# Kernel optimization log

Measured on AMD Instinct MI355X. Metric: run time of the kernel, lower is better.

Reference implementation:

```python
import jax, jax.numpy as jnp
import numpy as np

N = 50000
E = 800000
D_IN = 128
D_HID = 128
D_EMB = 128
N_CLS = 3
EPS = 0.0  # GINConv default eps, not trainable here
LRELU_SLOPE = 0.2


def setup_inputs() -> dict:
    key = jax.random.key(0)
    ks = jax.random.split(key, 12)
    x = jax.random.normal(ks[0], (N, D_IN), dtype=jnp.float32)
    edge_index = jax.random.randint(ks[1], (2, E), 0, N, dtype=jnp.int64)
    node_label = jnp.zeros((10000, 1, N_CLS), dtype=jnp.float32)
    node_index = jax.random.randint(ks[2], (10000,), 0, N, dtype=jnp.int64)
    def lin(k, fan_in, fan_out):
        kw, kb = jax.random.split(k)
        bound = 1.0 / np.sqrt(fan_in)
        W = jax.random.uniform(kw, (fan_out, fan_in), minval=-bound, maxval=bound, dtype=jnp.float32)
        b = jax.random.uniform(kb, (fan_out,), minval=-bound, maxval=bound, dtype=jnp.float32)
        return W, b
    W1, b1 = lin(ks[3], D_IN, D_HID)
    W2, b2 = lin(ks[4], D_HID, D_HID)
    W3, b3 = lin(ks[5], D_HID, D_EMB)
    Wout, bout = lin(ks[6], D_EMB, N_CLS)
    return {"x": x, "edge_index": edge_index, "node_label": node_label,
            "node_index": node_index, "W1": W1, "b1": b1, "W2": W2, "b2": b2,
            "W3": W3, "b3": b3, "Wout": Wout, "bout": bout}


def gin_conv(x, src, dst, W, b):
    # h = Linear(x); out = relu(scatter_add(h[src] -> dst) + (1+eps)*h)
    h = x @ W.T + b                                   # [N, F_out]
    agg = jax.ops.segment_sum(h[src], dst, num_segments=N)
    return jax.nn.relu(agg + (1.0 + EPS) * h)


def leaky_relu(x):
    return jnp.where(x >= 0, x, LRELU_SLOPE * x)


def reference(x, edge_index, node_label, node_index, W1, b1, W2, b2, W3, b3, Wout, bout):
    src, dst = edge_index[0], edge_index[1]
    h = leaky_relu(gin_conv(x, src, dst, W1, b1))
    h = leaky_relu(gin_conv(h, src, dst, W2, b2))
    h = leaky_relu(gin_conv(h, src, dst, W3, b3))
    x_embed = h                                       # [N, D_EMB]
    output = h @ Wout.T + bout                        # [N, N_CLS]
    node_output = output[node_index]                  # [M, N_CLS]
    ypred = jnp.argmax(output, axis=1)                # [N]
    y_nodepred = ypred[node_index]                    # [M]
    return (x_embed, node_output, ypred, y_nodepred)
```

## Files before the change

kernel.cpp:

```cpp
#include <hip/hip_runtime.h>

#define NN 50000
#define EE 800000
#define D 128
#define NCLS 3
#define MIDX 10000
#define NB 196
#define CHUNK 4096
#define HIST_WGS 98
#define WCONV_WGS 64
#define LIN1_WGS 782

typedef unsigned int uint32;
typedef unsigned short ushort16;
typedef __attribute__((ext_vector_type(8))) short short8;
typedef __attribute__((ext_vector_type(4))) float f32x4;

__device__ __forceinline__ ushort16 f2bf(float f) {
    uint32 u = __float_as_uint(f);
    u = (u + 0x7fffu + ((u >> 16) & 1u)) >> 16;
    return (ushort16)u;
}
__device__ __forceinline__ float bflo(uint32 packed) {
    return __uint_as_float(packed << 16);
}
__device__ __forceinline__ float bfhi(uint32 packed) {
    return __uint_as_float(packed & 0xFFFF0000u);
}

__device__ __forceinline__ void gather_rows(const uint32* __restrict__ h,
                                            const int* __restrict__ esrc,
                                            int beg, int end, int lane,
                                            float& a0, float& a1) {
    int i = beg;
    for (; i + 16 <= end; i += 16) {
        int s[16];
        uint32 q[16];
#pragma unroll
        for (int k = 0; k < 16; ++k) s[k] = esrc[i + k];
#pragma unroll
        for (int k = 0; k < 16; ++k) q[k] = h[(long long)s[k] * (D / 2) + lane];
        float t0a = 0.f, t0b = 0.f, t1a = 0.f, t1b = 0.f;
#pragma unroll
        for (int k = 0; k < 16; k += 2) {
            t0a += bflo(q[k]);     t1a += bfhi(q[k]);
            t0b += bflo(q[k + 1]); t1b += bfhi(q[k + 1]);
        }
        a0 += t0a + t0b;
        a1 += t1a + t1b;
    }
    for (; i + 4 <= end; i += 4) {
        int s[4];
        uint32 q[4];
#pragma unroll
        for (int k = 0; k < 4; ++k) s[k] = esrc[i + k];
#pragma unroll
        for (int k = 0; k < 4; ++k) q[k] = h[(long long)s[k] * (D / 2) + lane];
        a0 += (bflo(q[0]) + bflo(q[1])) + (bflo(q[2]) + bflo(q[3]));
        a1 += (bfhi(q[0]) + bfhi(q[1])) + (bfhi(q[2]) + bfhi(q[3]));
    }
    for (; i < end; ++i) {
        const uint32 q = h[(long long)esrc[i] * (D / 2) + lane];
        a0 += bflo(q);
        a1 += bfhi(q);
    }
}


__global__ __launch_bounds__(256) void prep_hist(const float* __restrict__ W1,
                                                 const float* __restrict__ W2,
                                                 const float* __restrict__ W3,
                                                 const int* __restrict__ dst,
                                                 ushort16* __restrict__ Wbf,
                                                 int* __restrict__ hpart) {
    const int t = threadIdx.x;
    if (blockIdx.x < WCONV_WGS) {
        const int i = blockIdx.x * 256 + t;
        Wbf[i] = f2bf(W1[i]);
        Wbf[i + D * D] = f2bf(W2[i]);
        Wbf[i + 2 * D * D] = f2bf(W3[i]);
    } else {
        __shared__ int hcnt[256];
        const int b = blockIdx.x - WCONV_WGS;
        hcnt[t] = 0;
        __syncthreads();
        const int e0 = b * 8192;
        const int e1 = (e0 + 8192 < EE) ? e0 + 8192 : EE;
        for (int s = e0 + t; s < e1; s += 256) atomicAdd(&hcnt[dst[s] >> 8], 1);
        __syncthreads();
        hpart[b * 256 + t] = hcnt[t];
    }
}


__global__ __launch_bounds__(256) void scan_linear1(const int* __restrict__ hpart,
                                                    int* __restrict__ bstart,
                                                    int* __restrict__ bcursor,
                                                    int* __restrict__ rowptr,
                                                    const float* __restrict__ x,
                                                    const ushort16* __restrict__ Wbf,
                                                    const float* __restrict__ bias,
                                                    ushort16* __restrict__ h) {
    if (blockIdx.x == 0) {
        __shared__ int s[256];
        const int t = threadIdx.x;
        int v = 0;
        if (t < NB)
            for (int w = 0; w < HIST_WGS; ++w) v += hpart[w * 256 + t];
        s[t] = v;
        __syncthreads();
        for (int off = 1; off < 256; off <<= 1) {
            const int add = (t >= off) ? s[t - off] : 0;
            __syncthreads();
            s[t] += add;
            __syncthreads();
        }
        const int excl = s[t] - v;
        if (t < NB) {
            bstart[t] = excl;
            bcursor[t * 16] = excl;
        }
        if (t == NB - 1) bstart[NB] = excl + v;
        if (t == 0) rowptr[NN] = EE;
        return;
    }
    const int wave = threadIdx.x >> 6;
    const int lane = threadIdx.x & 63;
    const int m0 = (blockIdx.x - 1) * 64 + wave * 16;
    if (m0 >= NN) return;
    const int lr = lane & 15;
    const int lk = (lane >> 4) * 8;

    f32x4 acc[8] = {};
#pragma unroll
    for (int k4 = 0; k4 < 4; ++k4) {
        const int kb = k4 * 32 + lk;
        const float4* xp = (const float4*)(x + (long long)(m0 + lr) * D + kb);
        const float4 a0 = xp[0];
        const float4 a1 = xp[1];
        short8 af;
        af[0] = (short)f2bf(a0.x); af[1] = (short)f2bf(a0.y);
        af[2] = (short)f2bf(a0.z); af[3] = (short)f2bf(a0.w);
        af[4] = (short)f2bf(a1.x); af[5] = (short)f2bf(a1.y);
        af[6] = (short)f2bf(a1.z); af[7] = (short)f2bf(a1.w);
#pragma unroll
        for (int nt = 0; nt < 8; ++nt) {
            const short8 bfrag = *(const short8*)(Wbf + (nt * 16 + lr) * D + kb);
            acc[nt] = __builtin_amdgcn_mfma_f32_16x16x32_bf16(af, bfrag, acc[nt], 0, 0, 0);
        }
    }
    const int rbase = m0 + (lane >> 4) * 4;
#pragma unroll
    for (int nt = 0; nt < 8; ++nt) {
        const int f = nt * 16 + lr;
        const float bb = bias[f];
#pragma unroll
        for (int r = 0; r < 4; ++r)
            h[(long long)(rbase + r) * D + f] = f2bf(acc[nt][r] + bb);
    }
}


__global__ __launch_bounds__(256) void fill_coarse(const int* __restrict__ src,
                                                   const int* __restrict__ dst,
                                                   int* __restrict__ bcursor,
                                                   int* __restrict__ espacked) {
    __shared__ int hcnt[256];
    __shared__ int hbase[256];
    const int t = threadIdx.x;
    const int e0 = blockIdx.x * CHUNK;
    const int e1 = (e0 + CHUNK < EE) ? e0 + CHUNK : EE;
    hcnt[t] = 0;
    __syncthreads();
    for (int s = e0 + t; s < e1; s += 256) atomicAdd(&hcnt[dst[s] >> 8], 1);
    __syncthreads();
    if (t < NB) {
        const int c = hcnt[t];
        hbase[t] = c ? atomicAdd(&bcursor[t * 16], c) : 0;
    }
    hcnt[t] = 0;
    __syncthreads();
    for (int s = e0 + t; s < e1; s += 256) {
        const int d = dst[s];
        const int b = d >> 8;
        const int r = atomicAdd(&hcnt[b], 1);
        espacked[hbase[b] + r] = (src[s] << 8) | (d & 255);
    }
}


__global__ __launch_bounds__(256) void bucket_scatter(const int* __restrict__ espacked,
                                                      const int* __restrict__ bstart,
                                                      int* __restrict__ rowptr,
                                                      int* __restrict__ esrc) {
    __shared__ int cnt[256];
    __shared__ int sc[256];
    __shared__ int cur[256];
    const int b = blockIdx.x;
    const int t = threadIdx.x;
    const int n0 = b * 256;
    const int seg0 = bstart[b];
    const int seg1 = bstart[b + 1];
    cnt[t] = 0;
    __syncthreads();
    for (int s = seg0 + t; s < seg1; s += 256) atomicAdd(&cnt[espacked[s] & 255], 1);
    __syncthreads();
    const int v = cnt[t];
    sc[t] = v;
    __syncthreads();
    for (int off = 1; off < 256; off <<= 1) {
        const int add = (t >= off) ? sc[t - off] : 0;
        __syncthreads();
        sc[t] += add;
        __syncthreads();
    }
    const int excl = seg0 + sc[t] - v;
    if (n0 + t < NN) rowptr[n0 + t] = excl;
    cur[t] = excl;
    __syncthreads();
    for (int s = seg0 + t; s < seg1; s += 256) {
        const int p = espacked[s];
        const int pos = atomicAdd(&cur[p & 255], 1);
        esrc[pos] = p >> 8;
    }
}


__global__ __launch_bounds__(256) void agg_linear(const uint32* __restrict__ h,
                                                  const int* __restrict__ rowptr,
                                                  const int* __restrict__ esrc,
                                                  const ushort16* __restrict__ Wbf,
                                                  const float* __restrict__ bias,
                                                  ushort16* __restrict__ hnext) {
    __shared__ uint32 xs[16][68];
    const int wave = threadIdx.x >> 6;
    const int lane = threadIdx.x & 63;
    const int m0 = blockIdx.x * 16;

#pragma unroll
    for (int j = 0; j < 4; ++j) {
        const int row = wave * 4 + j;
        const int node = __builtin_amdgcn_readfirstlane(m0 + row);
        const int beg = rowptr[node];
        const int end = rowptr[node + 1];
        const uint32 p = h[(long long)node * (D / 2) + lane];
        float acc0 = bflo(p), acc1 = bfhi(p);
        gather_rows(h, esrc, beg, end, lane, acc0, acc1);
        xs[row][lane] = ((uint32)f2bf(fmaxf(acc1, 0.f)) << 16) |
                        (uint32)f2bf(fmaxf(acc0, 0.f));
    }
    __syncthreads();

    const int lr = lane & 15;
    const int lk = (lane >> 4) * 8;
    f32x4 acc[2] = {};
#pragma unroll
    for (int k4 = 0; k4 < 4; ++k4) {
        const int kb = k4 * 32 + lk;
        const short8 af = *(const short8*)&xs[lr][kb >> 1];
#pragma unroll
        for (int f = 0; f < 2; ++f) {
            const int ft = wave * 2 + f;
            const short8 bfrag = *(const short8*)(Wbf + (ft * 16 + lr) * D + kb);
            acc[f] = __builtin_amdgcn_mfma_f32_16x16x32_bf16(af, bfrag, acc[f], 0, 0, 0);
        }
    }
    const int rbase = m0 + (lane >> 4) * 4;
#pragma unroll
    for (int f = 0; f < 2; ++f) {
        const int col = (wave * 2 + f) * 16 + lr;
        const float bb = bias[col];
#pragma unroll
        for (int r = 0; r < 4; ++r)
            hnext[(long long)(rbase + r) * D + col] = f2bf(acc[f][r] + bb);
    }
}


__global__ __launch_bounds__(256) void agg_head(const uint32* __restrict__ h,
                                                const int* __restrict__ rowptr,
                                                const int* __restrict__ esrc,
                                                float* __restrict__ xe,
                                                const float* __restrict__ Wout,
                                                const float* __restrict__ bout,
                                                float* __restrict__ logits,
                                                float* __restrict__ ypred) {
    const int wave = threadIdx.x >> 6;
    const int lane = threadIdx.x & 63;
    const int node = __builtin_amdgcn_readfirstlane(blockIdx.x * 4 + wave);
    if (node >= NN) return;
    const int beg = rowptr[node];
    const int end = rowptr[node + 1];
    const uint32 p = h[(long long)node * (D / 2) + lane];
    float acc0 = bflo(p), acc1 = bfhi(p);
    gather_rows(h, esrc, beg, end, lane, acc0, acc1);
    const float r0 = fmaxf(acc0, 0.f);
    const float r1 = fmaxf(acc1, 0.f);
    float2 r;
    r.x = r0;
    r.y = r1;
    ((float2*)(xe + (long long)node * D))[lane] = r;

    const float2 w0 = ((const float2*)(Wout + 0 * D))[lane];
    const float2 w1 = ((const float2*)(Wout + 1 * D))[lane];
    const float2 w2 = ((const float2*)(Wout + 2 * D))[lane];
    float l0 = r0 * w0.x + r1 * w0.y;
    float l1 = r0 * w1.x + r1 * w1.y;
    float l2 = r0 * w2.x + r1 * w2.y;
#pragma unroll
    for (int off = 32; off > 0; off >>= 1) {
        l0 += __shfl_xor(l0, off, 64);
        l1 += __shfl_xor(l1, off, 64);
        l2 += __shfl_xor(l2, off, 64);
    }
    if (lane == 0) {
        l0 += bout[0]; l1 += bout[1]; l2 += bout[2];
        logits[node * 3 + 0] = l0;
        logits[node * 3 + 1] = l1;
        logits[node * 3 + 2] = l2;
        int best = 0;
        float bv = l0;
        if (l1 > bv) { bv = l1; best = 1; }
        if (l2 > bv) { bv = l2; best = 2; }
        ypred[node] = (float)best;
    }
}


__global__ void gather_out(const float* __restrict__ logits, const float* __restrict__ ypred,
                           const int* __restrict__ nidx, float* __restrict__ node_out,
                           float* __restrict__ y_nodepred) {
    const int m = blockIdx.x * blockDim.x + threadIdx.x;
    if (m >= MIDX) return;
    const int n = nidx[m];
    node_out[m * 3 + 0] = logits[n * 3 + 0];
    node_out[m * 3 + 1] = logits[n * 3 + 1];
    node_out[m * 3 + 2] = logits[n * 3 + 2];
    y_nodepred[m] = ypred[n];
}

extern "C" void kernel_launch(void* const* d_in, const int* in_sizes, int n_in,
                              void* d_out, int out_size, void* d_ws, size_t ws_size,
                              hipStream_t stream) {
    const float* x0 = (const float*)d_in[0];
    const int* ei = (const int*)d_in[1];
    const int* src = ei;
    const int* dst = ei + EE;
    const int* nidx = (const int*)d_in[3];
    const float* W1 = (const float*)d_in[4];
    const float* b1 = (const float*)d_in[5];
    const float* W2 = (const float*)d_in[6];
    const float* b2 = (const float*)d_in[7];
    const float* W3 = (const float*)d_in[8];
    const float* b3 = (const float*)d_in[9];
    const float* Wout = (const float*)d_in[10];
    const float* bout = (const float*)d_in[11];

    char* ws = (char*)d_ws;
    ushort16* hbuf = (ushort16*)ws;
    ushort16* xbuf = hbuf + (long long)NN * D;
    ushort16* Wbf  = xbuf + (long long)NN * D;
    float* logits  = (float*)(Wbf + 3 * D * D);
    int* rowptr    = (int*)(logits + (long long)NN * NCLS);
    int* hpart     = rowptr + NN + 4;
    int* bstart    = hpart + HIST_WGS * 256;
    int* bcursor   = bstart + 256;
    int* espacked  = bcursor + NB * 16 + 12;
    int* esrc      = espacked + EE;

    float* out = (float*)d_out;
    float* xe       = out;
    float* node_out = out + (long long)NN * D;
    float* yp       = node_out + MIDX * NCLS;
    float* ynp      = yp + NN;

    prep_hist<<<WCONV_WGS + HIST_WGS, 256, 0, stream>>>(W1, W2, W3, dst, Wbf, hpart);
    scan_linear1<<<1 + LIN1_WGS, 256, 0, stream>>>(hpart, bstart, bcursor, rowptr,
                                                   x0, Wbf, b1, hbuf);
    fill_coarse<<<(EE + CHUNK - 1) / CHUNK, 256, 0, stream>>>(src, dst, bcursor, espacked);
    bucket_scatter<<<NB, 256, 0, stream>>>(espacked, bstart, rowptr, esrc);

    agg_linear<<<NN / 16, 256, 0, stream>>>((const uint32*)hbuf, rowptr, esrc,
                                            Wbf + (long long)D * D, b2, xbuf);
    agg_linear<<<NN / 16, 256, 0, stream>>>((const uint32*)xbuf, rowptr, esrc,
                                            Wbf + 2LL * D * D, b3, hbuf);
    agg_head<<<(NN + 3) / 4, 256, 0, stream>>>((const uint32*)hbuf, rowptr, esrc,
                                               xe, Wout, bout, logits, yp);
    gather_out<<<(MIDX + 255) / 256, 256, 0, stream>>>(logits, yp, nidx, node_out, ynp);
}
```

Baseline: 180.3 us.

## Fuse bucket scan into consumers and merge scatter with first linear layer

Replaces the per-workgroup histogram partials and the standalone scan kernel with global atomic bucket counts. fill_coarse and the scatter blocks each rescan those counts redundantly in shared memory. The bucket scatter is merged into the same launch as the first linear layer, which cuts one kernel launch and one dependency stage from the preprocessing chain. The cost is a memset launch to zero the counters and cursors, plus a 196-entry scan repeated in every block.

```diff
diff --git a/kernel.cpp b/kernel.cpp
--- a/kernel.cpp
+++ b/kernel.cpp
@@ -9,6 +9,7 @@
 #define CHUNK 4096
 #define HIST_WGS 98
 #define WCONV_WGS 64
+#define SCAT_WGS NB
 #define LIN1_WGS 782
 
 typedef unsigned int uint32;
@@ -66,13 +67,26 @@
     }
 }
 
+__device__ __forceinline__ void bucket_scan(const int* __restrict__ gbucket,
+                                            int* sc, int t, int& v) {
+    v = (t < NB) ? gbucket[t] : 0;
+    sc[t] = v;
+    __syncthreads();
+    for (int off = 1; off < 256; off <<= 1) {
+        const int add = (t >= off) ? sc[t - off] : 0;
+        __syncthreads();
+        sc[t] += add;
+        __syncthreads();
+    }
+}
+
 
 __global__ __launch_bounds__(256) void prep_hist(const float* __restrict__ W1,
                                                  const float* __restrict__ W2,
                                                  const float* __restrict__ W3,
                                                  const int* __restrict__ dst,
                                                  ushort16* __restrict__ Wbf,
-                                                 int* __restrict__ hpart) {
+                                                 int* __restrict__ gbucket) {
     const int t = threadIdx.x;
     if (blockIdx.x < WCONV_WGS) {
         const int i = blockIdx.x * 256 + t;
@@ -88,45 +102,97 @@
         const int e1 = (e0 + 8192 < EE) ? e0 + 8192 : EE;
         for (int s = e0 + t; s < e1; s += 256) atomicAdd(&hcnt[dst[s] >> 8], 1);
         __syncthreads();
-        hpart[b * 256 + t] = hcnt[t];
-    }
-}
-
-
-__global__ __launch_bounds__(256) void scan_linear1(const int* __restrict__ hpart,
-                                                    int* __restrict__ bstart,
-                                                    int* __restrict__ bcursor,
-                                                    int* __restrict__ rowptr,
-                                                    const float* __restrict__ x,
-                                                    const ushort16* __restrict__ Wbf,
-                                                    const float* __restrict__ bias,
-                                                    ushort16* __restrict__ h) {
-    if (blockIdx.x == 0) {
-        __shared__ int s[256];
-        const int t = threadIdx.x;
-        int v = 0;
-        if (t < NB)
-            for (int w = 0; w < HIST_WGS; ++w) v += hpart[w * 256 + t];
-        s[t] = v;
+        if (t < NB && hcnt[t]) atomicAdd(&gbucket[t], hcnt[t]);
+    }
+}
+
+
+__global__ __launch_bounds__(256) void fill_coarse(const int* __restrict__ src,
+                                                   const int* __restrict__ dst,
+                                                   const int* __restrict__ gbucket,
+                                                   int* __restrict__ bcursor,
+                                                   int* __restrict__ espacked) {
+    __shared__ int sc[256];
+    __shared__ int hcnt[256];
+    __shared__ int hbase[256];
+    const int t = threadIdx.x;
+    int v;
+    bucket_scan(gbucket, sc, t, v);
+    const int bstart_t = sc[t] - v;
+    const int e0 = blockIdx.x * CHUNK;
+    const int e1 = (e0 + CHUNK < EE) ? e0 + CHUNK : EE;
+    hcnt[t] = 0;
+    __syncthreads();
+    for (int s = e0 + t; s < e1; s += 256) atomicAdd(&hcnt[dst[s] >> 8], 1);
+    __syncthreads();
+    if (t < NB) {
+        const int c = hcnt[t];
+        hbase[t] = c ? (bstart_t + atomicAdd(&bcursor[t * 16], c)) : 0;
+    }
+    hcnt[t] = 0;
+    __syncthreads();
+    for (int s = e0 + t; s < e1; s += 256) {
+        const int d = dst[s];
+        const int b = d >> 8;
+        const int r = atomicAdd(&hcnt[b], 1);
+        espacked[hbase[b] + r] = (src[s] << 8) | (d & 255);
+    }
+}
+
+
+__global__ __launch_bounds__(256) void scatter_linear1(const int* __restrict__ espacked,
+                                                       const int* __restrict__ gbucket,
+                                                       int* __restrict__ rowptr,
+                                                       int* __restrict__ esrc,
+                                                       const float* __restrict__ x,
+                                                       const ushort16* __restrict__ Wbf,
+                                                       const float* __restrict__ bias,
+                                                       ushort16* __restrict__ h) {
+    const int t = threadIdx.x;
+    if (blockIdx.x < SCAT_WGS) {
+        __shared__ int sc[256];
+        __shared__ int cnt[256];
+        __shared__ int cur[256];
+        __shared__ int segs[2];
+        const int b = blockIdx.x;
+        int v;
+        bucket_scan(gbucket, sc, t, v);
+        if (t == b) {
+            segs[0] = sc[t] - v;
+            segs[1] = sc[t];
+        }
+        __syncthreads();
+        const int seg0 = segs[0];
+        const int seg1 = segs[1];
+        const int n0 = b * 256;
+        cnt[t] = 0;
+        __syncthreads();
+        for (int s = seg0 + t; s < seg1; s += 256) atomicAdd(&cnt[espacked[s] & 255], 1);
+        __syncthreads();
+        const int c = cnt[t];
+        sc[t] = c;
         __syncthreads();
         for (int off = 1; off < 256; off <<= 1) {
-            const int add = (t >= off) ? s[t - off] : 0;
+            const int add = (t >= off) ? sc[t - off] : 0;
             __syncthreads();
-            s[t] += add;
+            sc[t] += add;
             __syncthreads();
         }
-        const int excl = s[t] - v;
-        if (t < NB) {
-            bstart[t] = excl;
-            bcursor[t * 16] = excl;
-        }
-        if (t == NB - 1) bstart[NB] = excl + v;
-        if (t == 0) rowptr[NN] = EE;
+        const int excl = seg0 + sc[t] - c;
+        if (n0 + t < NN) rowptr[n0 + t] = excl;
+        if (b == 0 && t == 0) rowptr[NN] = EE;
+        cur[t] = excl;
+        __syncthreads();
+        for (int s = seg0 + t; s < seg1; s += 256) {
+            const int p = espacked[s];
+            const int pos = atomicAdd(&cur[p & 255], 1);
+            esrc[pos] = p >> 8;
+        }
         return;
     }
-    const int wave = threadIdx.x >> 6;
-    const int lane = threadIdx.x & 63;
-    const int m0 = (blockIdx.x - 1) * 64 + wave * 16;
+    const int wave = t >> 6;
+    const int lane = t & 63;
+    const int m0 = (blockIdx.x - SCAT_WGS) * 64 + wave * 16;
     if (m0 >= NN) return;
     const int lr = lane & 15;
     const int lk = (lane >> 4) * 8;
@@ -157,71 +223,6 @@
 #pragma unroll
         for (int r = 0; r < 4; ++r)
             h[(long long)(rbase + r) * D + f] = f2bf(acc[nt][r] + bb);
-    }
-}
-
-
-__global__ __launch_bounds__(256) void fill_coarse(const int* __restrict__ src,
-                                                   const int* __restrict__ dst,
-                                                   int* __restrict__ bcursor,
-                                                   int* __restrict__ espacked) {
-    __shared__ int hcnt[256];
-    __shared__ int hbase[256];
-    const int t = threadIdx.x;
-    const int e0 = blockIdx.x * CHUNK;
-    const int e1 = (e0 + CHUNK < EE) ? e0 + CHUNK : EE;
-    hcnt[t] = 0;
-    __syncthreads();
-    for (int s = e0 + t; s < e1; s += 256) atomicAdd(&hcnt[dst[s] >> 8], 1);
-    __syncthreads();
-    if (t < NB) {
-        const int c = hcnt[t];
-        hbase[t] = c ? atomicAdd(&bcursor[t * 16], c) : 0;
-    }
-    hcnt[t] = 0;
-    __syncthreads();
-    for (int s = e0 + t; s < e1; s += 256) {
-        const int d = dst[s];
-        const int b = d >> 8;
-        const int r = atomicAdd(&hcnt[b], 1);
-        espacked[hbase[b] + r] = (src[s] << 8) | (d & 255);
-    }
-}
-
-
-__global__ __launch_bounds__(256) void bucket_scatter(const int* __restrict__ espacked,
-                                                      const int* __restrict__ bstart,
-                                                      int* __restrict__ rowptr,
-                                                      int* __restrict__ esrc) {
-    __shared__ int cnt[256];
-    __shared__ int sc[256];
-    __shared__ int cur[256];
-    const int b = blockIdx.x;
-    const int t = threadIdx.x;
-    const int n0 = b * 256;
-    const int seg0 = bstart[b];
-    const int seg1 = bstart[b + 1];
-    cnt[t] = 0;
-    __syncthreads();
-    for (int s = seg0 + t; s < seg1; s += 256) atomicAdd(&cnt[espacked[s] & 255], 1);
-    __syncthreads();
-    const int v = cnt[t];
-    sc[t] = v;
-    __syncthreads();
-    for (int off = 1; off < 256; off <<= 1) {
-        const int add = (t >= off) ? sc[t - off] : 0;
-        __syncthreads();
-        sc[t] += add;
-        __syncthreads();
-    }
-    const int excl = seg0 + sc[t] - v;
-    if (n0 + t < NN) rowptr[n0 + t] = excl;
-    cur[t] = excl;
-    __syncthreads();
-    for (int s = seg0 + t; s < seg1; s += 256) {
-        const int p = espacked[s];
-        const int pos = atomicAdd(&cur[p & 255], 1);
-        esrc[pos] = p >> 8;
     }
 }
 
@@ -362,9 +363,8 @@
     ushort16* Wbf  = xbuf + (long long)NN * D;
     float* logits  = (float*)(Wbf + 3 * D * D);
     int* rowptr    = (int*)(logits + (long long)NN * NCLS);
-    int* hpart     = rowptr + NN + 4;
-    int* bstart    = hpart + HIST_WGS * 256;
-    int* bcursor   = bstart + 256;
+    int* gbucket   = rowptr + NN + 4;
+    int* bcursor   = gbucket + 256;
     int* espacked  = bcursor + NB * 16 + 12;
     int* esrc      = espacked + EE;
 
@@ -374,11 +374,13 @@
     float* yp       = node_out + MIDX * NCLS;
     float* ynp      = yp + NN;
 
-    prep_hist<<<WCONV_WGS + HIST_WGS, 256, 0, stream>>>(W1, W2, W3, dst, Wbf, hpart);
-    scan_linear1<<<1 + LIN1_WGS, 256, 0, stream>>>(hpart, bstart, bcursor, rowptr,
-                                                   x0, Wbf, b1, hbuf);
-    fill_coarse<<<(EE + CHUNK - 1) / CHUNK, 256, 0, stream>>>(src, dst, bcursor, espacked);
-    bucket_scatter<<<NB, 256, 0, stream>>>(espacked, bstart, rowptr, esrc);
+    hipMemsetAsync(gbucket, 0, (256 + NB * 16 + 12) * sizeof(int), stream);
+
+    prep_hist<<<WCONV_WGS + HIST_WGS, 256, 0, stream>>>(W1, W2, W3, dst, Wbf, gbucket);
+    fill_coarse<<<(EE + CHUNK - 1) / CHUNK, 256, 0, stream>>>(src, dst, gbucket,
+                                                              bcursor, espacked);
+    scatter_linear1<<<SCAT_WGS + LIN1_WGS, 256, 0, stream>>>(espacked, gbucket, rowptr,
+                                                             esrc, x0, Wbf, b1, hbuf);
 
     agg_linear<<<NN / 16, 256, 0, stream>>>((const uint32*)hbuf, rowptr, esrc,
                                             Wbf + (long long)D * D, b2, xbuf);
```

New measurement: 174.8 us. -3.1%, faster.
